# Kernel optimization log

Measured on AMD Instinct MI355X. Metric: run time of the kernel, lower is better.

Reference implementation:

```python
import jax, jax.numpy as jnp
import numpy as np

B, S, D, H = 2, 2048, 1024, 16
DK = D // H


def setup_inputs() -> dict:
    key = jax.random.key(0)
    ks = jax.random.split(key, 11)
    scale = 1.0 / np.sqrt(D)
    inp = {
        "q": jax.random.normal(ks[0], (B, S, D), jnp.float32),
        "k": jax.random.normal(ks[1], (B, S, D), jnp.float32),
        "v": jax.random.normal(ks[2], (B, S, D), jnp.float32),
        "mask": jnp.tril(jnp.ones((S, S), jnp.int32))[None, None],  # causal [1,1,S,S]
        "wq": jax.random.normal(ks[3], (D, D), jnp.float32) * scale,
        "bq": jnp.zeros((D,), jnp.float32),
        "wk": jax.random.normal(ks[4], (D, D), jnp.float32) * scale,
        "bk": jnp.zeros((D,), jnp.float32),
        "wv": jax.random.normal(ks[5], (D, D), jnp.float32) * scale,
        "bv": jnp.zeros((D,), jnp.float32),
        "wo": jax.random.normal(ks[6], (D, D), jnp.float32) * scale,
        "bo": jnp.zeros((D,), jnp.float32),
    }
    return inp


def _split_heads(x):  # [B,S,D] -> [B,H,S,DK]
    return x.reshape(B, S, H, DK).transpose(0, 2, 1, 3)


def reference(q, k, v, mask, wq, bq, wk, bk, wv, bv, wo, bo):
    # projections (nn.Linear: x @ W.T + b)
    query = _split_heads(q @ wq.T + bq)
    key_ = _split_heads(k @ wk.T + bk)
    value = _split_heads(v @ wv.T + bv)
    # scaled dot-product attention, full [B,H,S,S] scores as in source
    scores = jnp.einsum('bhqd,bhkd->bhqk', query, key_) / np.sqrt(DK)
    scores = jnp.where(mask == 0, jnp.float32(-1e9), scores)
    attn = jax.nn.softmax(scores, axis=-1)
    out = jnp.einsum('bhqk,bhkd->bhqd', attn, value)
    out = out.transpose(0, 2, 1, 3).reshape(B, S, D)
    x = out @ wo.T + bo
    return x, attn
```

## Files before the change

### kernel.cpp

```cpp
#include <hip/hip_runtime.h>
#include <hip/hip_bf16.h>

typedef __attribute__((ext_vector_type(8))) __bf16 bf16x8;
typedef __attribute__((ext_vector_type(4))) __bf16 bf16x4;
typedef __attribute__((ext_vector_type(4))) float f32x4;

#define MFMA16(a, b, c) __builtin_amdgcn_mfma_f32_16x16x32_bf16((a), (b), (c), 0, 0, 0)

#define SEQ 2048
#define DIM 1024

__global__ __launch_bounds__(256) void qkv_gemm(
    const float* __restrict__ qI, const float* __restrict__ kI, const float* __restrict__ vI,
    const float* __restrict__ wqI, const float* __restrict__ wkI, const float* __restrict__ wvI,
    const float* __restrict__ bqI, const float* __restrict__ bkI, const float* __restrict__ bvI,
    __bf16* __restrict__ Qp, __bf16* __restrict__ Kp, __bf16* __restrict__ Vp) {
  const int N = 1024, K = 1024;
  int z = blockIdx.z;
  const float* A = (z == 0) ? qI : (z == 1) ? kI : vI;
  const float* W = (z == 0) ? wqI : (z == 1) ? wkI : wvI;
  const float* bias = (z == 0) ? bqI : (z == 1) ? bkI : bvI;
  __bf16* C = (z == 0) ? Qp : (z == 1) ? Kp : Vp;

  __shared__ __bf16 As[128][40];
  __shared__ __bf16 Bs[128][40];

  int tid = threadIdx.x;
  int wave = tid >> 6, lane = tid & 63;
  int quad = lane >> 4, l16 = lane & 15;
  int wm = (wave >> 1) * 64, wn = (wave & 1) * 64;
  int m0 = blockIdx.y * 128, n0 = blockIdx.x * 128;
  int sr = tid >> 3;
  int sc = (tid & 7) * 4;

  f32x4 acc[4][4] = {};

  for (int k0 = 0; k0 < K; k0 += 32) {
    __syncthreads();
#pragma unroll
    for (int i = 0; i < 4; i++) {
      int r = sr + i * 32;
      float4 av = *(const float4*)&A[(size_t)(m0 + r) * K + k0 + sc];
      float4 wv4 = *(const float4*)&W[(size_t)(n0 + r) * K + k0 + sc];
      bf16x4 ah = {(__bf16)av.x, (__bf16)av.y, (__bf16)av.z, (__bf16)av.w};
      bf16x4 wh = {(__bf16)wv4.x, (__bf16)wv4.y, (__bf16)wv4.z, (__bf16)wv4.w};
      *(bf16x4*)&As[r][sc] = ah;
      *(bf16x4*)&Bs[r][sc] = wh;
    }
    __syncthreads();
    bf16x8 af[4], bfv[4];
#pragma unroll
    for (int i = 0; i < 4; i++) af[i] = *(bf16x8*)&As[wm + i * 16 + l16][quad * 8];
#pragma unroll
    for (int j = 0; j < 4; j++) bfv[j] = *(bf16x8*)&Bs[wn + j * 16 + l16][quad * 8];
#pragma unroll
    for (int i = 0; i < 4; i++)
#pragma unroll
      for (int j = 0; j < 4; j++) acc[i][j] = MFMA16(af[i], bfv[j], acc[i][j]);
  }

#pragma unroll
  for (int j = 0; j < 4; j++) {
    int col = n0 + wn + j * 16 + l16;
    float bj = bias[col];
#pragma unroll
    for (int i = 0; i < 4; i++)
#pragma unroll
      for (int r = 0; r < 4; r++) {
        int row = m0 + wm + i * 16 + quad * 4 + r;
        C[(size_t)row * N + col] = (__bf16)(acc[i][j][r] + bj);
      }
  }
}

__global__ __launch_bounds__(256) void out_gemm(
    const __bf16* __restrict__ A, const float* __restrict__ W,
    const float* __restrict__ bias, float* __restrict__ C) {
  const int N = 1024, K = 1024;
  __shared__ __bf16 As[128][40];
  __shared__ __bf16 Bs[128][40];

  int tid = threadIdx.x;
  int wave = tid >> 6, lane = tid & 63;
  int quad = lane >> 4, l16 = lane & 15;
  int wm = (wave >> 1) * 64, wn = (wave & 1) * 64;
  int m0 = blockIdx.y * 128, n0 = blockIdx.x * 128;
  int sr = tid >> 3;
  int sc = (tid & 7) * 4;

  f32x4 acc[4][4] = {};

  for (int k0 = 0; k0 < K; k0 += 32) {
    __syncthreads();
#pragma unroll
    for (int i = 0; i < 4; i++) {
      int r = sr + i * 32;
      bf16x4 ah = *(const bf16x4*)&A[(size_t)(m0 + r) * K + k0 + sc];
      float4 wv4 = *(const float4*)&W[(size_t)(n0 + r) * K + k0 + sc];
      bf16x4 wh = {(__bf16)wv4.x, (__bf16)wv4.y, (__bf16)wv4.z, (__bf16)wv4.w};
      *(bf16x4*)&As[r][sc] = ah;
      *(bf16x4*)&Bs[r][sc] = wh;
    }
    __syncthreads();
    bf16x8 af[4], bfv[4];
#pragma unroll
    for (int i = 0; i < 4; i++) af[i] = *(bf16x8*)&As[wm + i * 16 + l16][quad * 8];
#pragma unroll
    for (int j = 0; j < 4; j++) bfv[j] = *(bf16x8*)&Bs[wn + j * 16 + l16][quad * 8];
#pragma unroll
    for (int i = 0; i < 4; i++)
#pragma unroll
      for (int j = 0; j < 4; j++) acc[i][j] = MFMA16(af[i], bfv[j], acc[i][j]);
  }

#pragma unroll
  for (int j = 0; j < 4; j++) {
    int col = n0 + wn + j * 16 + l16;
    float bj = bias[col];
#pragma unroll
    for (int i = 0; i < 4; i++)
#pragma unroll
      for (int r = 0; r < 4; r++) {
        int row = m0 + wm + i * 16 + quad * 4 + r;
        C[(size_t)row * N + col] = acc[i][j][r] + bj;
      }
  }
}

__global__ __launch_bounds__(256) void attn_fused(
    const __bf16* __restrict__ Qp, const __bf16* __restrict__ Kp,
    const __bf16* __restrict__ Vp, float* __restrict__ attn,
    __bf16* __restrict__ Oc) {
  int bh = blockIdx.y;
  int b = bh >> 4;
  int hofs = (bh & 15) * 64;
  int q0 = blockIdx.x * 64;

  int tid = threadIdx.x;
  int wave = tid >> 6, lane = tid & 63;
  int quad = lane >> 4, l16 = lane & 15;

  __shared__ __bf16 Qs[64][72];
  __shared__ __bf16 Ks[128][72];
  __shared__ __bf16 Vts[64][136];
  __shared__ __bf16 Ps[64][136];

  const size_t rowbase = (size_t)b * SEQ;

#pragma unroll
  for (int it = 0; it < 2; it++) {
    int flat = tid * 8 + it * 2048;
    int r = flat >> 6, c = flat & 63;
    bf16x8 qv = *(const bf16x8*)&Qp[(rowbase + q0 + r) * DIM + hofs + c];
    *(bf16x8*)&Qs[r][c] = qv;
  }

  int myrow = q0 + wave * 16 + quad * 4;
  float m_i[4], l_i[4];
#pragma unroll
  for (int r = 0; r < 4; r++) { m_i[r] = -1e30f; l_i[r] = 0.f; }

  int ktmax = (q0 + 63) >> 7;

  for (int kt = 0; kt <= ktmax; kt++) {
    int k0 = kt << 7;
    __syncthreads();
#pragma unroll
    for (int it = 0; it < 4; it++) {
      int flat = tid * 8 + it * 2048;
      int r = flat >> 6, c = flat & 63;
      bf16x8 kv = *(const bf16x8*)&Kp[(rowbase + k0 + r) * DIM + hofs + c];
      *(bf16x8*)&Ks[r][c] = kv;
    }
    __syncthreads();

    f32x4 sacc[8] = {};
#pragma unroll
    for (int ks = 0; ks < 2; ks++) {
      bf16x8 a = *(bf16x8*)&Qs[wave * 16 + l16][ks * 32 + quad * 8];
#pragma unroll
      for (int t = 0; t < 8; t++) {
        bf16x8 bb = *(bf16x8*)&Ks[t * 16 + l16][ks * 32 + quad * 8];
        sacc[t] = MFMA16(a, bb, sacc[t]);
      }
    }
#pragma unroll
    for (int r = 0; r < 4; r++) {
      int rowr = myrow + r;
      float sv[8];
      float mx = -1e30f;
#pragma unroll
      for (int t = 0; t < 8; t++) {
        float s = sacc[t][r] * 0.125f;
        int col = k0 + t * 16 + l16;
        if (col > rowr) s = -1e30f;
        sv[t] = s;
        mx = fmaxf(mx, s);
      }
#pragma unroll
      for (int off = 1; off < 16; off <<= 1) mx = fmaxf(mx, __shfl_xor(mx, off));
      float mn = fmaxf(m_i[r], mx);
      float sum = 0.f;
#pragma unroll
      for (int t = 0; t < 8; t++) sum += __expf(sv[t] - mn);
#pragma unroll
      for (int off = 1; off < 16; off <<= 1) sum += __shfl_xor(sum, off);
      l_i[r] = l_i[r] * __expf(m_i[r] - mn) + sum;
      m_i[r] = mn;
    }
  }

  float rl[4];
#pragma unroll
  for (int r = 0; r < 4; r++) rl[r] = 1.f / l_i[r];

  f32x4 oacc[4] = {};
  float* attn_bh = attn + (size_t)bh * SEQ * SEQ;

  for (int kt = 0; kt < SEQ / 128; kt++) {
    int k0 = kt << 7;
    if (kt <= ktmax) {
      __syncthreads();
#pragma unroll
      for (int it = 0; it < 4; it++) {
        int flat = tid * 8 + it * 2048;
        int r = flat >> 6, c = flat & 63;
        bf16x8 kv = *(const bf16x8*)&Kp[(rowbase + k0 + r) * DIM + hofs + c];
        *(bf16x8*)&Ks[r][c] = kv;
        bf16x8 vv = *(const bf16x8*)&Vp[(rowbase + k0 + r) * DIM + hofs + c];
#pragma unroll
        for (int j = 0; j < 8; j++) Vts[c + j][r] = vv[j];
      }
      __syncthreads();

      f32x4 sacc[8] = {};
#pragma unroll
      for (int ks = 0; ks < 2; ks++) {
        bf16x8 a = *(bf16x8*)&Qs[wave * 16 + l16][ks * 32 + quad * 8];
#pragma unroll
        for (int t = 0; t < 8; t++) {
          bf16x8 bb = *(bf16x8*)&Ks[t * 16 + l16][ks * 32 + quad * 8];
          sacc[t] = MFMA16(a, bb, sacc[t]);
        }
      }
#pragma unroll
      for (int r = 0; r < 4; r++) {
        int rowr = myrow + r;
        size_t arow = (size_t)rowr * SEQ;
#pragma unroll
        for (int t = 0; t < 8; t++) {
          int col = k0 + t * 16 + l16;
          float s = sacc[t][r] * 0.125f;
          float p = (col <= rowr) ? __expf(s - m_i[r]) * rl[r] : 0.f;
          attn_bh[arow + col] = p;
          Ps[wave * 16 + quad * 4 + r][t * 16 + l16] = (__bf16)p;
        }
      }
      __syncthreads();
#pragma unroll
      for (int ks = 0; ks < 4; ks++) {
        bf16x8 a = *(bf16x8*)&Ps[wave * 16 + l16][ks * 32 + quad * 8];
#pragma unroll
        for (int dt = 0; dt < 4; dt++) {
          bf16x8 bb = *(bf16x8*)&Vts[dt * 16 + l16][ks * 32 + quad * 8];
          oacc[dt] = MFMA16(a, bb, oacc[dt]);
        }
      }
    } else {
      float4 z4 = make_float4(0.f, 0.f, 0.f, 0.f);
#pragma unroll
      for (int i = 0; i < 8; i++) {
        int f4 = tid + i * 256;
        int r = f4 >> 5;
        int c = (f4 & 31) * 4;
        *(float4*)&attn_bh[(size_t)(q0 + r) * SEQ + k0 + c] = z4;
      }
    }
  }

#pragma unroll
  for (int dt = 0; dt < 4; dt++)
#pragma unroll
    for (int r = 0; r < 4; r++) {
      int row = myrow + r;
      int col = hofs + dt * 16 + l16;
      Oc[(rowbase + row) * DIM + col] = (__bf16)oacc[dt][r];
    }
}

extern "C" void kernel_launch(void* const* d_in, const int* in_sizes, int n_in,
                              void* d_out, int out_size, void* d_ws, size_t ws_size,
                              hipStream_t stream) {
  const float* q = (const float*)d_in[0];
  const float* k = (const float*)d_in[1];
  const float* v = (const float*)d_in[2];
  const float* wq = (const float*)d_in[4];
  const float* bq = (const float*)d_in[5];
  const float* wk = (const float*)d_in[6];
  const float* bk = (const float*)d_in[7];
  const float* wv = (const float*)d_in[8];
  const float* bv = (const float*)d_in[9];
  const float* wo = (const float*)d_in[10];
  const float* bo = (const float*)d_in[11];

  float* xout = (float*)d_out;
  float* attn = xout + (size_t)2 * SEQ * DIM;

  __bf16* Qp = (__bf16*)d_ws;
  __bf16* Kp = Qp + (size_t)2 * SEQ * DIM;
  __bf16* Vp = Kp + (size_t)2 * SEQ * DIM;
  __bf16* Oc = Vp + (size_t)2 * SEQ * DIM;

  dim3 blk(256);
  dim3 g1(8, 32, 3);
  qkv_gemm<<<g1, blk, 0, stream>>>(q, k, v, wq, wk, wv, bq, bk, bv, Qp, Kp, Vp);

  dim3 g2(32, 32);
  attn_fused<<<g2, blk, 0, stream>>>(Qp, Kp, Vp, attn, Oc);

  dim3 g3(8, 32);
  out_gemm<<<g3, blk, 0, stream>>>(Oc, wo, bo, xout);
}
```

Baseline: 833.5 us.

## Transpose V in projection epilogue, swap QK operands for row-contiguous softmax and attn stores

```diff
diff --git a/kernel.cpp b/kernel.cpp
--- a/kernel.cpp
+++ b/kernel.cpp
@@ -14,13 +14,12 @@
     const float* __restrict__ qI, const float* __restrict__ kI, const float* __restrict__ vI,
     const float* __restrict__ wqI, const float* __restrict__ wkI, const float* __restrict__ wvI,
     const float* __restrict__ bqI, const float* __restrict__ bkI, const float* __restrict__ bvI,
-    __bf16* __restrict__ Qp, __bf16* __restrict__ Kp, __bf16* __restrict__ Vp) {
+    __bf16* __restrict__ Qp, __bf16* __restrict__ Kp, __bf16* __restrict__ Vt) {
   const int N = 1024, K = 1024;
   int z = blockIdx.z;
   const float* A = (z == 0) ? qI : (z == 1) ? kI : vI;
   const float* W = (z == 0) ? wqI : (z == 1) ? wkI : wvI;
   const float* bias = (z == 0) ? bqI : (z == 1) ? bkI : bvI;
-  __bf16* C = (z == 0) ? Qp : (z == 1) ? Kp : Vp;
 
   __shared__ __bf16 As[128][40];
   __shared__ __bf16 Bs[128][40];
@@ -35,19 +34,33 @@
 
   f32x4 acc[4][4] = {};
 
+  float4 pa[4], pw[4];
+#pragma unroll
+  for (int i = 0; i < 4; i++) {
+    int r = sr + i * 32;
+    pa[i] = *(const float4*)&A[(size_t)(m0 + r) * K + sc];
+    pw[i] = *(const float4*)&W[(size_t)(n0 + r) * K + sc];
+  }
+
   for (int k0 = 0; k0 < K; k0 += 32) {
     __syncthreads();
 #pragma unroll
     for (int i = 0; i < 4; i++) {
       int r = sr + i * 32;
-      float4 av = *(const float4*)&A[(size_t)(m0 + r) * K + k0 + sc];
-      float4 wv4 = *(const float4*)&W[(size_t)(n0 + r) * K + k0 + sc];
-      bf16x4 ah = {(__bf16)av.x, (__bf16)av.y, (__bf16)av.z, (__bf16)av.w};
-      bf16x4 wh = {(__bf16)wv4.x, (__bf16)wv4.y, (__bf16)wv4.z, (__bf16)wv4.w};
+      bf16x4 ah = {(__bf16)pa[i].x, (__bf16)pa[i].y, (__bf16)pa[i].z, (__bf16)pa[i].w};
+      bf16x4 wh = {(__bf16)pw[i].x, (__bf16)pw[i].y, (__bf16)pw[i].z, (__bf16)pw[i].w};
       *(bf16x4*)&As[r][sc] = ah;
       *(bf16x4*)&Bs[r][sc] = wh;
     }
     __syncthreads();
+    if (k0 + 32 < K) {
+#pragma unroll
+      for (int i = 0; i < 4; i++) {
+        int r = sr + i * 32;
+        pa[i] = *(const float4*)&A[(size_t)(m0 + r) * K + k0 + 32 + sc];
+        pw[i] = *(const float4*)&W[(size_t)(n0 + r) * K + k0 + 32 + sc];
+      }
+    }
     bf16x8 af[4], bfv[4];
 #pragma unroll
     for (int i = 0; i < 4; i++) af[i] = *(bf16x8*)&As[wm + i * 16 + l16][quad * 8];
@@ -63,13 +76,26 @@
   for (int j = 0; j < 4; j++) {
     int col = n0 + wn + j * 16 + l16;
     float bj = bias[col];
-#pragma unroll
-    for (int i = 0; i < 4; i++)
-#pragma unroll
-      for (int r = 0; r < 4; r++) {
-        int row = m0 + wm + i * 16 + quad * 4 + r;
-        C[(size_t)row * N + col] = (__bf16)(acc[i][j][r] + bj);
-      }
+    if (z == 2) {
+#pragma unroll
+      for (int i = 0; i < 4; i++) {
+        int row0 = m0 + wm + i * 16 + quad * 4;
+        int bb = row0 >> 11, s = row0 & 2047;
+        bf16x4 pv = {(__bf16)(acc[i][j][0] + bj), (__bf16)(acc[i][j][1] + bj),
+                     (__bf16)(acc[i][j][2] + bj), (__bf16)(acc[i][j][3] + bj)};
+        *(bf16x4*)&Vt[((size_t)bb * 1024 + col) * SEQ + s] = pv;
+      }
+    } else {
+      __bf16* C = (z == 0) ? Qp : Kp;
+      float scale = (z == 0) ? 0.125f : 1.0f;
+#pragma unroll
+      for (int i = 0; i < 4; i++)
+#pragma unroll
+        for (int r = 0; r < 4; r++) {
+          int row = m0 + wm + i * 16 + quad * 4 + r;
+          C[(size_t)row * N + col] = (__bf16)((acc[i][j][r] + bj) * scale);
+        }
+    }
   }
 }
 
@@ -90,18 +116,33 @@
 
   f32x4 acc[4][4] = {};
 
+  bf16x4 pa[4];
+  float4 pw[4];
+#pragma unroll
+  for (int i = 0; i < 4; i++) {
+    int r = sr + i * 32;
+    pa[i] = *(const bf16x4*)&A[(size_t)(m0 + r) * K + sc];
+    pw[i] = *(const float4*)&W[(size_t)(n0 + r) * K + sc];
+  }
+
   for (int k0 = 0; k0 < K; k0 += 32) {
     __syncthreads();
 #pragma unroll
     for (int i = 0; i < 4; i++) {
       int r = sr + i * 32;
-      bf16x4 ah = *(const bf16x4*)&A[(size_t)(m0 + r) * K + k0 + sc];
-      float4 wv4 = *(const float4*)&W[(size_t)(n0 + r) * K + k0 + sc];
-      bf16x4 wh = {(__bf16)wv4.x, (__bf16)wv4.y, (__bf16)wv4.z, (__bf16)wv4.w};
-      *(bf16x4*)&As[r][sc] = ah;
+      bf16x4 wh = {(__bf16)pw[i].x, (__bf16)pw[i].y, (__bf16)pw[i].z, (__bf16)pw[i].w};
+      *(bf16x4*)&As[r][sc] = pa[i];
       *(bf16x4*)&Bs[r][sc] = wh;
     }
     __syncthreads();
+    if (k0 + 32 < K) {
+#pragma unroll
+      for (int i = 0; i < 4; i++) {
+        int r = sr + i * 32;
+        pa[i] = *(const bf16x4*)&A[(size_t)(m0 + r) * K + k0 + 32 + sc];
+        pw[i] = *(const float4*)&W[(size_t)(n0 + r) * K + k0 + 32 + sc];
+      }
+    }
     bf16x8 af[4], bfv[4];
 #pragma unroll
     for (int i = 0; i < 4; i++) af[i] = *(bf16x8*)&As[wm + i * 16 + l16][quad * 8];
@@ -129,7 +170,7 @@
 
 __global__ __launch_bounds__(256) void attn_fused(
     const __bf16* __restrict__ Qp, const __bf16* __restrict__ Kp,
-    const __bf16* __restrict__ Vp, float* __restrict__ attn,
+    const __bf16* __restrict__ Vt, float* __restrict__ attn,
     __bf16* __restrict__ Oc) {
   int bh = blockIdx.y;
   int b = bh >> 4;
@@ -146,20 +187,21 @@
   __shared__ __bf16 Ps[64][136];
 
   const size_t rowbase = (size_t)b * SEQ;
+  const size_t vtbase = (size_t)bh * 64 * SEQ;
 
 #pragma unroll
   for (int it = 0; it < 2; it++) {
     int flat = tid * 8 + it * 2048;
     int r = flat >> 6, c = flat & 63;
-    bf16x8 qv = *(const bf16x8*)&Qp[(rowbase + q0 + r) * DIM + hofs + c];
-    *(bf16x8*)&Qs[r][c] = qv;
-  }
-
-  int myrow = q0 + wave * 16 + quad * 4;
-  float m_i[4], l_i[4];
-#pragma unroll
-  for (int r = 0; r < 4; r++) { m_i[r] = -1e30f; l_i[r] = 0.f; }
-
+    *(bf16x8*)&Qs[r][c] = *(const bf16x8*)&Qp[(rowbase + q0 + r) * DIM + hofs + c];
+  }
+  __syncthreads();
+
+  int qg = q0 + wave * 16 + l16;
+  bf16x8 qfrag0 = *(bf16x8*)&Qs[wave * 16 + l16][quad * 8];
+  bf16x8 qfrag1 = *(bf16x8*)&Qs[wave * 16 + l16][32 + quad * 8];
+
+  float m_i = -1e30f, l_i = 0.f;
   int ktmax = (q0 + 63) >> 7;
 
   for (int kt = 0; kt <= ktmax; kt++) {
@@ -169,53 +211,48 @@
     for (int it = 0; it < 4; it++) {
       int flat = tid * 8 + it * 2048;
       int r = flat >> 6, c = flat & 63;
-      bf16x8 kv = *(const bf16x8*)&Kp[(rowbase + k0 + r) * DIM + hofs + c];
-      *(bf16x8*)&Ks[r][c] = kv;
+      *(bf16x8*)&Ks[r][c] = *(const bf16x8*)&Kp[(rowbase + k0 + r) * DIM + hofs + c];
     }
     __syncthreads();
 
     f32x4 sacc[8] = {};
 #pragma unroll
-    for (int ks = 0; ks < 2; ks++) {
-      bf16x8 a = *(bf16x8*)&Qs[wave * 16 + l16][ks * 32 + quad * 8];
-#pragma unroll
-      for (int t = 0; t < 8; t++) {
-        bf16x8 bb = *(bf16x8*)&Ks[t * 16 + l16][ks * 32 + quad * 8];
-        sacc[t] = MFMA16(a, bb, sacc[t]);
-      }
-    }
-#pragma unroll
-    for (int r = 0; r < 4; r++) {
-      int rowr = myrow + r;
-      float sv[8];
-      float mx = -1e30f;
-#pragma unroll
-      for (int t = 0; t < 8; t++) {
-        float s = sacc[t][r] * 0.125f;
-        int col = k0 + t * 16 + l16;
-        if (col > rowr) s = -1e30f;
-        sv[t] = s;
+    for (int t = 0; t < 8; t++) {
+      bf16x8 a0 = *(bf16x8*)&Ks[t * 16 + l16][quad * 8];
+      bf16x8 a1 = *(bf16x8*)&Ks[t * 16 + l16][32 + quad * 8];
+      sacc[t] = MFMA16(a0, qfrag0, sacc[t]);
+      sacc[t] = MFMA16(a1, qfrag1, sacc[t]);
+    }
+
+    bool diag = (kt == ktmax);
+    float sv[32];
+    float mx = -1e30f;
+#pragma unroll
+    for (int t = 0; t < 8; t++)
+#pragma unroll
+      for (int r = 0; r < 4; r++) {
+        float s = sacc[t][r];
+        int k = k0 + t * 16 + quad * 4 + r;
+        if (diag && k > qg) s = -1e30f;
+        sv[t * 4 + r] = s;
         mx = fmaxf(mx, s);
       }
-#pragma unroll
-      for (int off = 1; off < 16; off <<= 1) mx = fmaxf(mx, __shfl_xor(mx, off));
-      float mn = fmaxf(m_i[r], mx);
-      float sum = 0.f;
-#pragma unroll
-      for (int t = 0; t < 8; t++) sum += __expf(sv[t] - mn);
-#pragma unroll
-      for (int off = 1; off < 16; off <<= 1) sum += __shfl_xor(sum, off);
-      l_i[r] = l_i[r] * __expf(m_i[r] - mn) + sum;
-      m_i[r] = mn;
-    }
-  }
-
-  float rl[4];
-#pragma unroll
-  for (int r = 0; r < 4; r++) rl[r] = 1.f / l_i[r];
-
+    mx = fmaxf(mx, __shfl_xor(mx, 16));
+    mx = fmaxf(mx, __shfl_xor(mx, 32));
+    float mn = fmaxf(m_i, mx);
+    float sum = 0.f;
+#pragma unroll
+    for (int i = 0; i < 32; i++) sum += __expf(sv[i] - mn);
+    sum += __shfl_xor(sum, 16);
+    sum += __shfl_xor(sum, 32);
+    l_i = l_i * __expf(m_i - mn) + sum;
+    m_i = mn;
+  }
+
+  float rl = 1.f / l_i;
   f32x4 oacc[4] = {};
   float* attn_bh = attn + (size_t)bh * SEQ * SEQ;
+  float* attn_row = attn_bh + (size_t)qg * SEQ;
 
   for (int kt = 0; kt < SEQ / 128; kt++) {
     int k0 = kt << 7;
@@ -225,38 +262,37 @@
       for (int it = 0; it < 4; it++) {
         int flat = tid * 8 + it * 2048;
         int r = flat >> 6, c = flat & 63;
-        bf16x8 kv = *(const bf16x8*)&Kp[(rowbase + k0 + r) * DIM + hofs + c];
-        *(bf16x8*)&Ks[r][c] = kv;
-        bf16x8 vv = *(const bf16x8*)&Vp[(rowbase + k0 + r) * DIM + hofs + c];
-#pragma unroll
-        for (int j = 0; j < 8; j++) Vts[c + j][r] = vv[j];
+        *(bf16x8*)&Ks[r][c] = *(const bf16x8*)&Kp[(rowbase + k0 + r) * DIM + hofs + c];
+        int d = flat >> 7, c2 = flat & 127;
+        *(bf16x8*)&Vts[d][c2] = *(const bf16x8*)&Vt[vtbase + (size_t)d * SEQ + k0 + c2];
       }
       __syncthreads();
 
       f32x4 sacc[8] = {};
 #pragma unroll
-      for (int ks = 0; ks < 2; ks++) {
-        bf16x8 a = *(bf16x8*)&Qs[wave * 16 + l16][ks * 32 + quad * 8];
-#pragma unroll
-        for (int t = 0; t < 8; t++) {
-          bf16x8 bb = *(bf16x8*)&Ks[t * 16 + l16][ks * 32 + quad * 8];
-          sacc[t] = MFMA16(a, bb, sacc[t]);
+      for (int t = 0; t < 8; t++) {
+        bf16x8 a0 = *(bf16x8*)&Ks[t * 16 + l16][quad * 8];
+        bf16x8 a1 = *(bf16x8*)&Ks[t * 16 + l16][32 + quad * 8];
+        sacc[t] = MFMA16(a0, qfrag0, sacc[t]);
+        sacc[t] = MFMA16(a1, qfrag1, sacc[t]);
+      }
+
+      bool diag = (kt == ktmax);
+#pragma unroll
+      for (int t = 0; t < 8; t++) {
+        float p[4];
+#pragma unroll
+        for (int r = 0; r < 4; r++) {
+          int k = k0 + t * 16 + quad * 4 + r;
+          float s = sacc[t][r];
+          p[r] = (!diag || k <= qg) ? __expf(s - m_i) * rl : 0.f;
         }
-      }
-#pragma unroll
-      for (int r = 0; r < 4; r++) {
-        int rowr = myrow + r;
-        size_t arow = (size_t)rowr * SEQ;
-#pragma unroll
-        for (int t = 0; t < 8; t++) {
-          int col = k0 + t * 16 + l16;
-          float s = sacc[t][r] * 0.125f;
-          float p = (col <= rowr) ? __expf(s - m_i[r]) * rl[r] : 0.f;
-          attn_bh[arow + col] = p;
-          Ps[wave * 16 + quad * 4 + r][t * 16 + l16] = (__bf16)p;
-        }
+        *(float4*)&attn_row[k0 + t * 16 + quad * 4] = make_float4(p[0], p[1], p[2], p[3]);
+        bf16x4 ph = {(__bf16)p[0], (__bf16)p[1], (__bf16)p[2], (__bf16)p[3]};
+        *(bf16x4*)&Ps[wave * 16 + l16][t * 16 + quad * 4] = ph;
       }
       __syncthreads();
+
 #pragma unroll
       for (int ks = 0; ks < 4; ks++) {
         bf16x8 a = *(bf16x8*)&Ps[wave * 16 + l16][ks * 32 + quad * 8];
@@ -281,10 +317,9 @@
 #pragma unroll
   for (int dt = 0; dt < 4; dt++)
 #pragma unroll
-    for (int r = 0; r < 4; r++) {
-      int row = myrow + r;
-      int col = hofs + dt * 16 + l16;
-      Oc[(rowbase + row) * DIM + col] = (__bf16)oacc[dt][r];
+    for (int rr = 0; rr < 4; rr++) {
+      int row = q0 + wave * 16 + quad * 4 + rr;
+      Oc[(rowbase + row) * DIM + hofs + dt * 16 + l16] = (__bf16)oacc[dt][rr];
     }
 }
 
@@ -308,15 +343,15 @@
 
   __bf16* Qp = (__bf16*)d_ws;
   __bf16* Kp = Qp + (size_t)2 * SEQ * DIM;
-  __bf16* Vp = Kp + (size_t)2 * SEQ * DIM;
-  __bf16* Oc = Vp + (size_t)2 * SEQ * DIM;
+  __bf16* Vt = Kp + (size_t)2 * SEQ * DIM;
+  __bf16* Oc = Vt + (size_t)2 * SEQ * DIM;
 
   dim3 blk(256);
   dim3 g1(8, 32, 3);
-  qkv_gemm<<<g1, blk, 0, stream>>>(q, k, v, wq, wk, wv, bq, bk, bv, Qp, Kp, Vp);
+  qkv_gemm<<<g1, blk, 0, stream>>>(q, k, v, wq, wk, wv, bq, bk, bv, Qp, Kp, Vt);
 
   dim3 g2(32, 32);
-  attn_fused<<<g2, blk, 0, stream>>>(Qp, Kp, Vp, attn, Oc);
+  attn_fused<<<g2, blk, 0, stream>>>(Qp, Kp, Vt, attn, Oc);
 
   dim3 g3(8, 32);
   out_gemm<<<g3, blk, 0, stream>>>(Oc, wo, bo, xout);
```

Measured after the change: 793.3 us. -4.8%, faster.
